# Performance work log

Hardware: AMD Instinct MI355X
Metric: run time of the kernel (lower is better)

The kernel has to match this reference:

```python
import jax, jax.numpy as jnp
import numpy as np

N_NODES = 50000
N_EDGES = 800000
F_IN = 64
HID = 64
N_GRAPHS = 256
BN_EPS = 1e-5


def setup_inputs() -> dict:
    key = jax.random.key(0)
    ks = jax.random.split(key, 16)
    inp = {
        'x': jax.random.normal(ks[0], (N_NODES, F_IN), dtype=jnp.float32),
        'edge_index': jax.random.randint(ks[1], (2, N_EDGES), 0, N_NODES, dtype=jnp.int64),
        'edge_weight': jax.random.uniform(ks[2], (N_EDGES,), dtype=jnp.float32),
        'batch': jnp.sort(jax.random.randint(ks[3], (N_NODES,), 0, N_GRAPHS, dtype=jnp.int64)),
    }
    def lin(k, fi, fo):
        s = 1.0 / np.sqrt(fi)
        kw, kb = jax.random.split(k)
        return (jax.random.uniform(kw, (fi, fo), jnp.float32, -s, s),
                jax.random.uniform(kb, (fo,), jnp.float32, -s, s))
    inp['W1'], inp['b1'] = lin(ks[4], F_IN, HID)
    inp['W2'], inp['b2'] = lin(ks[5], HID, HID)
    inp['W3'], inp['b3'] = lin(ks[6], HID, HID)
    inp['fcW1'], inp['fcb1'] = lin(ks[7], HID, HID)
    inp['fcW2'], inp['fcb2'] = lin(ks[8], HID, 1)
    for i, k in zip((1, 2, 3), ks[9:12]):
        inp[f'g{i}'] = jnp.ones((HID,), jnp.float32)
        inp[f'be{i}'] = jnp.zeros((HID,), jnp.float32)
    return inp


def gin_conv(x, src, dst, edge_weight, W, b):
    # weighted scatter-add aggregation: agg[dst] += w_e * x[src]
    msg = x[src] * edge_weight[:, None]            # [E, d]
    agg = jax.ops.segment_sum(msg, dst, num_segments=x.shape[0])  # [N, d]
    return (x + agg) @ W + b                       # GIN eps=0, nn = Linear


def batch_norm(x, gamma, beta):
    mu = jnp.mean(x, axis=0)
    var = jnp.var(x, axis=0)
    return (x - mu) * jax.lax.rsqrt(var + BN_EPS) * gamma + beta


def reference(x, edge_index, edge_weight, batch,
              W1, b1, W2, b2, W3, b3, fcW1, fcb1, fcW2, fcb2,
              g1, be1, g2, be2, g3, be3):
    src, dst = edge_index[0], edge_index[1]
    h = batch_norm(jax.nn.relu(gin_conv(x, src, dst, edge_weight, W1, b1)), g1, be1)
    h = batch_norm(jax.nn.relu(gin_conv(h, src, dst, edge_weight, W2, b2)), g2, be2)
    h = batch_norm(gin_conv(h, src, dst, edge_weight, W3, b3), g3, be3)
    pooled = jax.ops.segment_sum(h, batch, num_segments=N_GRAPHS)  # global_add_pool
    h = jax.nn.relu(pooled)
    h = jax.nn.relu(h @ fcW1 + fcb1)
    # dropout is identity in eval / deterministic reference
    return (h @ fcW2 + fcb2).reshape(-1)
```

## Files before the change

kernel.cpp:

```cpp
#include <hip/hip_runtime.h>
#include <hip/hip_bf16.h>


#define NN 50000
#define NE 800000
#define FD 64
#define NG 256
#define CAP 64
#define BN_EPS 1e-5f

#define NPART 8
#define PSIZE 6250
#define ECHUNK 2048
#define NCHUNK ((NE + ECHUNK - 1) / ECHUNK)
#define NBUILD (NCHUNK * NPART)
#define NCVT   ((NN * 16) / 256)

__device__ __forceinline__ float4 dec4(uint2 a) {
    float4 f;
    f.x = __uint_as_float(a.x << 16);
    f.y = __uint_as_float(a.x & 0xFFFF0000u);
    f.z = __uint_as_float(a.y << 16);
    f.w = __uint_as_float(a.y & 0xFFFF0000u);
    return f;
}
__device__ __forceinline__ unsigned rbf(float f) {
    unsigned u = __float_as_uint(f);
    return (u + 0x7FFFu + ((u >> 16) & 1u)) >> 16;
}
__device__ __forceinline__ uint2 enc4(float4 v) {
    uint2 o;
    o.x = rbf(v.x) | (rbf(v.y) << 16);
    o.y = rbf(v.z) | (rbf(v.w) << 16);
    return o;
}

__global__ __launch_bounds__(256) void build_cvt_kernel(
    const int* __restrict__ src, const int* __restrict__ dst,
    const float* __restrict__ ew, int* __restrict__ cursor,
    unsigned* __restrict__ slots,
    const float4* __restrict__ xin, uint2* __restrict__ xout)
{
    int bid = blockIdx.x;
    int tid = threadIdx.x;
    if (bid < NBUILD) {
        int part  = bid & 7;
        int chunk = bid >> 3;
        int base  = chunk * ECHUNK;
        #pragma unroll
        for (int i = 0; i < ECHUNK; i += 256) {
            int e = base + i + tid;
            if (e < NE) {
                int d = dst[e];
                if (d / PSIZE == part) {
                    int pos = atomicAdd(&cursor[d], 1) & (CAP - 1);
                    slots[(size_t)d * CAP + pos] =
                        ((unsigned)src[e] << 16) | rbf(ew[e]);
                }
            }
        }
    } else {
        int i = (bid - NBUILD) * 256 + tid;
        xout[i] = enc4(xin[i]);
    }
}

__global__ __launch_bounds__(256) void agg_layer_kernel(
    const uint2* __restrict__ h, const int* __restrict__ deg,
    const unsigned* __restrict__ slots,
    const float* __restrict__ prev_buckets,
    const float* __restrict__ prev_gamma, const float* __restrict__ prev_beta,
    const float* __restrict__ W, const float* __restrict__ b,
    uint2* __restrict__ y, float* __restrict__ buckets, int relu_flag)
{
    __shared__ float Ws[FD * FD];
    __shared__ float ps1[4][FD];
    __shared__ float ps2[4][FD];
    __shared__ float afs[FD], cfs[FD];
    int tid  = threadIdx.x;
    int wave = tid >> 6, lane = tid & 63;
    int g = lane >> 4, l = lane & 15;
    int node = blockIdx.x * 4 + wave;

    {
        float4* Wv = (float4*)Ws;
        const float4* Wg = (const float4*)W;
        #pragma unroll
        for (int i = 0; i < 4; i++) Wv[tid + 256 * i] = Wg[tid + 256 * i];
    }

    unsigned ms = slots[(size_t)node * CAP + lane];
    int dg = deg[node];
    float4 self = dec4(h[(size_t)node * 16 + l]);
    if (dg > CAP) dg = CAP;

    if (prev_buckets) {
        int f = tid & 63, q = tid >> 6;
        float S1 = 0.f, S2 = 0.f;
        #pragma unroll
        for (int i = 0; i < 16; i++) {
            int bkt = q * 16 + i;
            S1 += prev_buckets[bkt * 128 + f];
            S2 += prev_buckets[bkt * 128 + FD + f];
        }
        ps1[q][f] = S1;
        ps2[q][f] = S2;
    }
    __syncthreads();
    if (prev_buckets && tid < FD) {
        float s1 = ps1[0][tid] + ps1[1][tid] + ps1[2][tid] + ps1[3][tid];
        float s2 = ps2[0][tid] + ps2[1][tid] + ps2[2][tid] + ps2[3][tid];
        float mu  = s1 * (1.f / NN);
        float var = s2 * (1.f / NN) - mu * mu;
        float a = prev_gamma[tid] * rsqrtf(var + BN_EPS);
        afs[tid] = a;
        cfs[tid] = prev_beta[tid] - mu * a;
    }
    __syncthreads();

    float4 af = make_float4(1.f, 1.f, 1.f, 1.f);
    float4 cf = make_float4(0.f, 0.f, 0.f, 0.f);
    if (prev_buckets) {
        af = ((const float4*)afs)[l];
        cf = ((const float4*)cfs)[l];
    }

    float4 acc = make_float4(0.f, 0.f, 0.f, 0.f);
    float wsum = 0.f;
    if (dg <= 16) {
        unsigned m[4]; float w[4]; uint2 r[4];
        #pragma unroll
        for (int j = 0; j < 4; j++) {
            int e = 4 * j + g;
            int ee = (e < dg) ? e : 0;
            m[j] = (unsigned)__shfl((int)ms, ee, 64);
            float wj = __uint_as_float(m[j] << 16);
            w[j] = (e < dg) ? wj : 0.f;
        }
        #pragma unroll
        for (int j = 0; j < 4; j++)
            r[j] = h[(size_t)(m[j] >> 16) * 16 + l];
        #pragma unroll
        for (int j = 0; j < 4; j++) {
            float4 v = dec4(r[j]);
            wsum += w[j];
            acc.x = fmaf(w[j], v.x, acc.x); acc.y = fmaf(w[j], v.y, acc.y);
            acc.z = fmaf(w[j], v.z, acc.z); acc.w = fmaf(w[j], v.w, acc.w);
        }
    } else {
        int nIter = (dg + 31) >> 5;
        for (int i = 0; i < nIter; i++) {
            unsigned m[8]; float w[8]; uint2 r[8];
            #pragma unroll
            for (int j = 0; j < 8; j++) {
                int e = 32 * i + 4 * j + g;
                int ee = (e < dg) ? e : 0;
                m[j] = (unsigned)__shfl((int)ms, ee, 64);
                float wj = __uint_as_float(m[j] << 16);
                w[j] = (e < dg) ? wj : 0.f;
            }
            #pragma unroll
            for (int j = 0; j < 8; j++)
                r[j] = h[(size_t)(m[j] >> 16) * 16 + l];
            #pragma unroll
            for (int j = 0; j < 8; j++) {
                float4 v = dec4(r[j]);
                wsum += w[j];
                acc.x = fmaf(w[j], v.x, acc.x); acc.y = fmaf(w[j], v.y, acc.y);
                acc.z = fmaf(w[j], v.z, acc.z); acc.w = fmaf(w[j], v.w, acc.w);
            }
        }
    }
    acc.x += __shfl_xor(acc.x, 16, 64); acc.y += __shfl_xor(acc.y, 16, 64);
    acc.z += __shfl_xor(acc.z, 16, 64); acc.w += __shfl_xor(acc.w, 16, 64);
    wsum  += __shfl_xor(wsum, 16, 64);
    acc.x += __shfl_xor(acc.x, 32, 64); acc.y += __shfl_xor(acc.y, 32, 64);
    acc.z += __shfl_xor(acc.z, 32, 64); acc.w += __shfl_xor(acc.w, 32, 64);
    wsum  += __shfl_xor(wsum, 32, 64);

    float4 raw;
    raw.x = self.x + acc.x; raw.y = self.y + acc.y;
    raw.z = self.z + acc.z; raw.w = self.w + acc.w;

    float sw = 1.0f + wsum;
    float4 hin;
    hin.x = fmaf(af.x, raw.x, cf.x * sw);
    hin.y = fmaf(af.y, raw.y, cf.y * sw);
    hin.z = fmaf(af.z, raw.z, cf.z * sw);
    hin.w = fmaf(af.w, raw.w, cf.w * sw);

    const float4* __restrict__ WsV = (const float4*)Ws;
    float4 yp = make_float4(0.f, 0.f, 0.f, 0.f);
    #pragma unroll
    for (int kk = 0; kk < 4; kk++) {
        int srcl = 4 * g + kk;
        float a0 = __shfl(hin.x, srcl, 64);
        float a1 = __shfl(hin.y, srcl, 64);
        float a2 = __shfl(hin.z, srcl, 64);
        float a3 = __shfl(hin.w, srcl, 64);
        int k0 = 16 * g + 4 * kk;
        float4 w0 = WsV[(k0 + 0) * 16 + l];
        float4 w1 = WsV[(k0 + 1) * 16 + l];
        float4 w2 = WsV[(k0 + 2) * 16 + l];
        float4 w3 = WsV[(k0 + 3) * 16 + l];
        yp.x = fmaf(a0, w0.x, yp.x); yp.y = fmaf(a0, w0.y, yp.y);
        yp.z = fmaf(a0, w0.z, yp.z); yp.w = fmaf(a0, w0.w, yp.w);
        yp.x = fmaf(a1, w1.x, yp.x); yp.y = fmaf(a1, w1.y, yp.y);
        yp.z = fmaf(a1, w1.z, yp.z); yp.w = fmaf(a1, w1.w, yp.w);
        yp.x = fmaf(a2, w2.x, yp.x); yp.y = fmaf(a2, w2.y, yp.y);
        yp.z = fmaf(a2, w2.z, yp.z); yp.w = fmaf(a2, w2.w, yp.w);
        yp.x = fmaf(a3, w3.x, yp.x); yp.y = fmaf(a3, w3.y, yp.y);
        yp.z = fmaf(a3, w3.z, yp.z); yp.w = fmaf(a3, w3.w, yp.w);
    }
    yp.x += __shfl_xor(yp.x, 16, 64); yp.y += __shfl_xor(yp.y, 16, 64);
    yp.z += __shfl_xor(yp.z, 16, 64); yp.w += __shfl_xor(yp.w, 16, 64);
    yp.x += __shfl_xor(yp.x, 32, 64); yp.y += __shfl_xor(yp.y, 32, 64);
    yp.z += __shfl_xor(yp.z, 32, 64); yp.w += __shfl_xor(yp.w, 32, 64);

    float4 bias = ((const float4*)b)[l];
    float4 yv;
    yv.x = yp.x + bias.x; yv.y = yp.y + bias.y;
    yv.z = yp.z + bias.z; yv.w = yp.w + bias.w;
    if (relu_flag) {
        yv.x = fmaxf(yv.x, 0.f); yv.y = fmaxf(yv.y, 0.f);
        yv.z = fmaxf(yv.z, 0.f); yv.w = fmaxf(yv.w, 0.f);
    }
    if (g == 0) {
        y[(size_t)node * 16 + l] = enc4(yv);
        ((float4*)&ps1[wave][0])[l] = yv;
        float4 sq;
        sq.x = yv.x * yv.x; sq.y = yv.y * yv.y;
        sq.z = yv.z * yv.z; sq.w = yv.w * yv.w;
        ((float4*)&ps2[wave][0])[l] = sq;
    }
    __syncthreads();
    if (tid < FD) {
        float a = ps1[0][tid] + ps1[1][tid] + ps1[2][tid] + ps1[3][tid];
        float q = ps2[0][tid] + ps2[1][tid] + ps2[2][tid] + ps2[3][tid];
        float* bk = buckets + (blockIdx.x & 63) * 128;
        atomicAdd(&bk[tid], a);
        atomicAdd(&bk[FD + tid], q);
    }
}

__global__ __launch_bounds__(256) void pool_head_kernel(
    const uint2* __restrict__ y, const int* __restrict__ batch,
    const float* __restrict__ buckets3,
    const float* __restrict__ g3, const float* __restrict__ be3,
    const float* __restrict__ fcW1, const float* __restrict__ fcb1,
    const float* __restrict__ fcW2, const float* __restrict__ fcb2,
    float* __restrict__ out)
{
    __shared__ float red[16][FD];
    __shared__ float afs[FD], cfs[FD];
    __shared__ int bounds[2];
    int tid = threadIdx.x;
    int g = blockIdx.x;

    {
        int f = tid & 63, q = tid >> 6;
        float S1 = 0.f, S2 = 0.f;
        #pragma unroll
        for (int i = 0; i < 16; i++) {
            int bkt = q * 16 + i;
            S1 += buckets3[bkt * 128 + f];
            S2 += buckets3[bkt * 128 + FD + f];
        }
        red[q][f]     = S1;
        red[4 + q][f] = S2;
    }
    if (tid < 2) {
        int target = g + tid;
        int lo = 0, hi = NN;
        while (lo < hi) {
            int mid = (lo + hi) >> 1;
            if (batch[mid] < target) lo = mid + 1; else hi = mid;
        }
        bounds[tid] = lo;
    }
    __syncthreads();
    if (tid < FD) {
        float s1 = red[0][tid] + red[1][tid] + red[2][tid] + red[3][tid];
        float s2 = red[4][tid] + red[5][tid] + red[6][tid] + red[7][tid];
        float mu  = s1 * (1.f / NN);
        float var = s2 * (1.f / NN) - mu * mu;
        float a = g3[tid] * rsqrtf(var + BN_EPS);
        afs[tid] = a;
        cfs[tid] = be3[tid] - mu * a;
    }
    __syncthreads();

    int s = bounds[0], e = bounds[1];
    int l = tid & 15, r = tid >> 4;
    float4 acc = make_float4(0.f, 0.f, 0.f, 0.f);
    for (int n = s + r; n < e; n += 16) {
        float4 v = dec4(y[(size_t)n * 16 + l]);
        acc.x += v.x; acc.y += v.y; acc.z += v.z; acc.w += v.w;
    }
    ((float4*)&red[r][0])[l] = acc;
    __syncthreads();
    for (int off = 8; off > 0; off >>= 1) {
        if (r < off) {
            float4 a = ((float4*)&red[r][0])[l];
            float4 o = ((float4*)&red[r + off][0])[l];
            a.x += o.x; a.y += o.y; a.z += o.z; a.w += o.w;
            ((float4*)&red[r][0])[l] = a;
        }
        __syncthreads();
    }
    if (tid < 64) {
        float cnt = (float)(e - s);
        float p = red[0][tid];
        p = fmaf(afs[tid], p, cfs[tid] * cnt);
        p = fmaxf(p, 0.f);
        float acc1 = fcb1[tid];
        #pragma unroll
        for (int k = 0; k < FD; k++) {
            float pk = __shfl(p, k, 64);
            acc1 = fmaf(pk, fcW1[k * FD + tid], acc1);
        }
        acc1 = fmaxf(acc1, 0.f);
        float prod = acc1 * fcW2[tid];
        #pragma unroll
        for (int off = 32; off > 0; off >>= 1)
            prod += __shfl_xor(prod, off, 64);
        if (tid == 0) out[g] = prod + fcb2[0];
    }
}

extern "C" void kernel_launch(void* const* d_in, const int* in_sizes, int n_in,
                              void* d_out, int out_size, void* d_ws, size_t ws_size,
                              hipStream_t stream) {
    const float* x     = (const float*)d_in[0];
    const int*   ei    = (const int*)d_in[1];
    const float* ew    = (const float*)d_in[2];
    const int*   batch = (const int*)d_in[3];
    const float* W1 = (const float*)d_in[4],  *b1 = (const float*)d_in[5];
    const float* W2 = (const float*)d_in[6],  *b2 = (const float*)d_in[7];
    const float* W3 = (const float*)d_in[8],  *b3 = (const float*)d_in[9];
    const float* fcW1 = (const float*)d_in[10], *fcb1 = (const float*)d_in[11];
    const float* fcW2 = (const float*)d_in[12], *fcb2 = (const float*)d_in[13];
    const float* g1 = (const float*)d_in[14], *be1 = (const float*)d_in[15];
    const float* g2 = (const float*)d_in[16], *be2 = (const float*)d_in[17];
    const float* g3 = (const float*)d_in[18], *be3 = (const float*)d_in[19];
    float* out = (float*)d_out;

    const int* srcp = ei;
    const int* dstp = ei + NE;

    char* ws = (char*)d_ws;
    size_t off = 0;
    auto take = [&](size_t bytes) -> char* {
        char* p = ws + off;
        off += (bytes + 255) & ~(size_t)255;
        return p;
    };
    uint2*    xbf   = (uint2*)   take((size_t)NN * FD * 2);
    uint2*    bufA  = (uint2*)   take((size_t)NN * FD * 2);
    uint2*    bufB  = (uint2*)   take((size_t)NN * FD * 2);
    unsigned* slots = (unsigned*)take((size_t)NN * CAP * 4);
    size_t zero_base = off;
    int*      cursor= (int*)     take((size_t)NN * 4);
    float*    buckets=(float*)   take((size_t)3 * 64 * 128 * 4);
    size_t zero_bytes = off - zero_base;
    (void)ws_size; (void)n_in; (void)in_sizes; (void)out_size;

    hipMemsetAsync(ws + zero_base, 0, zero_bytes, stream);

    build_cvt_kernel<<<NBUILD + NCVT, 256, 0, stream>>>(srcp, dstp, ew,
                                                        cursor, slots,
                                                        (const float4*)x, xbf);

    const int gridA = NN / 4;

    float* bk1 = buckets + 0 * 64 * 128;
    float* bk2 = buckets + 1 * 64 * 128;
    float* bk3 = buckets + 2 * 64 * 128;

    agg_layer_kernel<<<gridA, 256, 0, stream>>>(xbf, cursor, slots,
                                                nullptr, nullptr, nullptr,
                                                W1, b1, bufA, bk1, 1);
    agg_layer_kernel<<<gridA, 256, 0, stream>>>(bufA, cursor, slots,
                                                bk1, g1, be1,
                                                W2, b2, bufB, bk2, 1);
    agg_layer_kernel<<<gridA, 256, 0, stream>>>(bufB, cursor, slots,
                                                bk2, g2, be2,
                                                W3, b3, bufA, bk3, 0);
    pool_head_kernel<<<NG, 256, 0, stream>>>(bufA, batch, bk3, g3, be3,
                                             fcW1, fcb1, fcW2, fcb2, out);
}
```

Before: 270.8 us.

## Zero-fill neighbor slots to drop edge masking and shrink BN stat buckets

The memset region now covers the slots array, so unused neighbor slots hold zero (weight 0, source node 0). That lets the gather loops skip the per-edge bounds check and the select on the weight. The number of atomic buckets for batch-norm statistics drops from 64 to 16, which cuts the reduction reads in later kernels but puts more atomic contention on each bucket. The cost is a much larger memset: about 12.8 MB more zeroing per call.

```diff
diff --git a/kernel.cpp b/kernel.cpp
--- a/kernel.cpp
+++ b/kernel.cpp
@@ -7,6 +7,7 @@
 #define FD 64
 #define NG 256
 #define CAP 64
+#define NBKT 16
 #define BN_EPS 1e-5f
 
 #define NPART 8
@@ -98,8 +99,8 @@
         int f = tid & 63, q = tid >> 6;
         float S1 = 0.f, S2 = 0.f;
         #pragma unroll
-        for (int i = 0; i < 16; i++) {
-            int bkt = q * 16 + i;
+        for (int i = 0; i < 4; i++) {
+            int bkt = q * 4 + i;
             S1 += prev_buckets[bkt * 128 + f];
             S2 += prev_buckets[bkt * 128 + FD + f];
         }
@@ -128,46 +129,38 @@
     float4 acc = make_float4(0.f, 0.f, 0.f, 0.f);
     float wsum = 0.f;
     if (dg <= 16) {
-        unsigned m[4]; float w[4]; uint2 r[4];
-        #pragma unroll
-        for (int j = 0; j < 4; j++) {
-            int e = 4 * j + g;
-            int ee = (e < dg) ? e : 0;
-            m[j] = (unsigned)__shfl((int)ms, ee, 64);
-            float wj = __uint_as_float(m[j] << 16);
-            w[j] = (e < dg) ? wj : 0.f;
-        }
+        unsigned m[4]; uint2 r[4];
+        #pragma unroll
+        for (int j = 0; j < 4; j++)
+            m[j] = (unsigned)__shfl((int)ms, 4 * j + g, 64);
         #pragma unroll
         for (int j = 0; j < 4; j++)
             r[j] = h[(size_t)(m[j] >> 16) * 16 + l];
         #pragma unroll
         for (int j = 0; j < 4; j++) {
+            float w = __uint_as_float(m[j] << 16);
             float4 v = dec4(r[j]);
-            wsum += w[j];
-            acc.x = fmaf(w[j], v.x, acc.x); acc.y = fmaf(w[j], v.y, acc.y);
-            acc.z = fmaf(w[j], v.z, acc.z); acc.w = fmaf(w[j], v.w, acc.w);
+            wsum += w;
+            acc.x = fmaf(w, v.x, acc.x); acc.y = fmaf(w, v.y, acc.y);
+            acc.z = fmaf(w, v.z, acc.z); acc.w = fmaf(w, v.w, acc.w);
         }
     } else {
         int nIter = (dg + 31) >> 5;
         for (int i = 0; i < nIter; i++) {
-            unsigned m[8]; float w[8]; uint2 r[8];
+            unsigned m[8]; uint2 r[8];
             #pragma unroll
-            for (int j = 0; j < 8; j++) {
-                int e = 32 * i + 4 * j + g;
-                int ee = (e < dg) ? e : 0;
-                m[j] = (unsigned)__shfl((int)ms, ee, 64);
-                float wj = __uint_as_float(m[j] << 16);
-                w[j] = (e < dg) ? wj : 0.f;
-            }
+            for (int j = 0; j < 8; j++)
+                m[j] = (unsigned)__shfl((int)ms, 32 * i + 4 * j + g, 64);
             #pragma unroll
             for (int j = 0; j < 8; j++)
                 r[j] = h[(size_t)(m[j] >> 16) * 16 + l];
             #pragma unroll
             for (int j = 0; j < 8; j++) {
+                float w = __uint_as_float(m[j] << 16);
                 float4 v = dec4(r[j]);
-                wsum += w[j];
-                acc.x = fmaf(w[j], v.x, acc.x); acc.y = fmaf(w[j], v.y, acc.y);
-                acc.z = fmaf(w[j], v.z, acc.z); acc.w = fmaf(w[j], v.w, acc.w);
+                wsum += w;
+                acc.x = fmaf(w, v.x, acc.x); acc.y = fmaf(w, v.y, acc.y);
+                acc.z = fmaf(w, v.z, acc.z); acc.w = fmaf(w, v.w, acc.w);
             }
         }
     }
@@ -237,7 +230,7 @@
     if (tid < FD) {
         float a = ps1[0][tid] + ps1[1][tid] + ps1[2][tid] + ps1[3][tid];
         float q = ps2[0][tid] + ps2[1][tid] + ps2[2][tid] + ps2[3][tid];
-        float* bk = buckets + (blockIdx.x & 63) * 128;
+        float* bk = buckets + (blockIdx.x & (NBKT - 1)) * 128;
         atomicAdd(&bk[tid], a);
         atomicAdd(&bk[FD + tid], q);
     }
@@ -261,8 +254,8 @@
         int f = tid & 63, q = tid >> 6;
         float S1 = 0.f, S2 = 0.f;
         #pragma unroll
-        for (int i = 0; i < 16; i++) {
-            int bkt = q * 16 + i;
+        for (int i = 0; i < 4; i++) {
+            int bkt = q * 4 + i;
             S1 += buckets3[bkt * 128 + f];
             S2 += buckets3[bkt * 128 + FD + f];
         }
@@ -358,10 +351,10 @@
     uint2*    xbf   = (uint2*)   take((size_t)NN * FD * 2);
     uint2*    bufA  = (uint2*)   take((size_t)NN * FD * 2);
     uint2*    bufB  = (uint2*)   take((size_t)NN * FD * 2);
+    size_t zero_base = off;
     unsigned* slots = (unsigned*)take((size_t)NN * CAP * 4);
-    size_t zero_base = off;
     int*      cursor= (int*)     take((size_t)NN * 4);
-    float*    buckets=(float*)   take((size_t)3 * 64 * 128 * 4);
+    float*    buckets=(float*)   take((size_t)3 * NBKT * 128 * 4);
     size_t zero_bytes = off - zero_base;
     (void)ws_size; (void)n_in; (void)in_sizes; (void)out_size;
 
@@ -373,9 +366,9 @@
 
     const int gridA = NN / 4;
 
-    float* bk1 = buckets + 0 * 64 * 128;
-    float* bk2 = buckets + 1 * 64 * 128;
-    float* bk3 = buckets + 2 * 64 * 128;
+    float* bk1 = buckets + 0 * NBKT * 128;
+    float* bk2 = buckets + 1 * NBKT * 128;
+    float* bk3 = buckets + 2 * NBKT * 128;
 
     agg_layer_kernel<<<gridA, 256, 0, stream>>>(xbf, cursor, slots,
                                                 nullptr, nullptr, nullptr,
```

After: 269.1 us. About the same (-0.6%).
